# Kernel tuning notes

Hardware: AMD Instinct MI355X
Metric: run time of the kernel (lower is better)

Reference implementation:

```python
import jax, jax.numpy as jnp
import numpy as np

B, S, D_IN, D_EMB, H = 2, 2048, 1024, 1024, 16
HD = D_EMB // H

def setup_inputs() -> dict:
    key = jax.random.key(0)
    k1, k2, k3 = jax.random.split(key, 3)
    # xavier-uniform style scales
    lim_qkv = float(np.sqrt(6.0 / (D_IN + 3 * D_EMB)))
    lim_o = float(np.sqrt(6.0 / (D_EMB + D_EMB)))
    return {
        "x": jax.random.normal(k1, (B, S, D_IN), dtype=jnp.float32),
        "W_qkv": jax.random.uniform(k2, (3 * D_EMB, D_IN), minval=-lim_qkv, maxval=lim_qkv, dtype=jnp.float32),
        "b_qkv": jnp.zeros((3 * D_EMB,), dtype=jnp.float32),
        "W_o": jax.random.uniform(k3, (D_EMB, D_EMB), minval=-lim_o, maxval=lim_o, dtype=jnp.float32),
        "b_o": jnp.zeros((D_EMB,), dtype=jnp.float32),
    }

def reference(x, W_qkv, b_qkv, W_o, b_o):
    b, s, _ = x.shape
    qkv = x @ W_qkv.T + b_qkv                     # [B,S,3E]
    qkv = qkv.reshape(b, s, H, 3 * HD).transpose(0, 2, 1, 3)  # [B,H,S,3*HD]
    q, k, v = jnp.split(qkv, 3, axis=-1)          # each [B,H,S,HD]
    scale = 1.0 / np.sqrt(HD)
    attn = jax.nn.softmax(jnp.einsum('bhqd,bhkd->bhqk', q, k) * scale, axis=-1)
    vals = jnp.einsum('bhqk,bhkd->bhqd', attn, v) # [B,H,S,HD]
    vals = vals.transpose(0, 2, 1, 3).reshape(b, s, D_EMB)
    return vals @ W_o.T + b_o
```

## Files before the change

kernel.cpp:

```cpp
#include <hip/hip_runtime.h>
#include <hip/hip_bf16.h>

typedef unsigned short u16;
typedef unsigned int u32;
typedef __bf16 bf16x8 __attribute__((ext_vector_type(8)));
typedef float f32x4 __attribute__((ext_vector_type(4)));
typedef u32 u32x4 __attribute__((ext_vector_type(4)));

#define MFMA16(a, b, c) __builtin_amdgcn_mfma_f32_16x16x32_bf16((a), (b), (c), 0, 0, 0)

static __device__ __forceinline__ u16 f2bf(float f) {
  __hip_bfloat16 h = __float2bfloat16(f);
  return __builtin_bit_cast(u16, h);
}

static __device__ __forceinline__ u32 pack2(float a, float b) {
  return (u32)f2bf(a) | ((u32)f2bf(b) << 16);
}

static __device__ __forceinline__ bf16x8 ldbf8(const void* p) {
  return *reinterpret_cast<const bf16x8*>(p);
}

static __device__ __forceinline__ void gload_lds16(const void* g, void* l) {
  __builtin_amdgcn_global_load_lds(
      (const __attribute__((address_space(1))) u32*)g,
      (__attribute__((address_space(3))) u32*)l, 16, 0, 0);
}

__global__ void cvt_all(const float* __restrict__ x, const float* __restrict__ wq,
                        const float* __restrict__ wo, u16* __restrict__ xb,
                        u16* __restrict__ wqb, u16* __restrict__ wob) {
  int i = blockIdx.x * 256 + threadIdx.x;
  const float* s;
  u16* d;
  int j;
  if (i < 524288) {
    s = x; d = xb; j = i;
  } else if (i < 917504) {
    s = wq; d = wqb; j = i - 524288;
  } else {
    s = wo; d = wob; j = i - 917504;
  }
  const float4* p = reinterpret_cast<const float4*>(s) + (size_t)j * 2;
  float4 a = p[0], b = p[1];
  uint4 o;
  o.x = (u32)f2bf(a.x) | ((u32)f2bf(a.y) << 16);
  o.y = (u32)f2bf(a.z) | ((u32)f2bf(a.w) << 16);
  o.z = (u32)f2bf(b.x) | ((u32)f2bf(b.y) << 16);
  o.w = (u32)f2bf(b.z) | ((u32)f2bf(b.w) << 16);
  reinterpret_cast<uint4*>(d)[j] = o;
}

template <bool BF16OUT>
__global__ __launch_bounds__(256, 3) void gemm_bt(const u16* __restrict__ A,
                                                  const u16* __restrict__ Bm,
                                                  const float* __restrict__ bias,
                                                  void* __restrict__ Cp,
                                                  int M, int N, int K) {
  __shared__ __align__(16) char As[128 * 64 * 2];
  __shared__ __align__(16) char Bs[128 * 64 * 2];
  const int tid = threadIdx.x;
  const int lane = tid & 63;
  const int wid = tid >> 6;
  const int fr = lane & 15, fg = lane >> 4;
  const int gx = gridDim.x, nwg = gx * gridDim.y;
  const int id = blockIdx.y * gx + blockIdx.x;
  const int nid = (id & 7) * (nwg >> 3) + (id >> 3);
  const int bm = nid / gx, bn = nid % gx;
  const int wm = (wid >> 1) * 64, wn = (wid & 1) * 64;

  f32x4 acc[4][4];
#pragma unroll
  for (int i = 0; i < 4; ++i)
#pragma unroll
    for (int j = 0; j < 4; ++j) acc[i][j] = (f32x4){0.f, 0.f, 0.f, 0.f};

  const int nk = K >> 6;
  for (int kt = 0; kt < nk; ++kt) {
#pragma unroll
    for (int it = 0; it < 4; ++it) {
      int q = it * 256 + tid;
      int row = q >> 3;
      int c = (q & 7) ^ (row & 7);
      gload_lds16(A + (size_t)(bm * 128 + row) * K + kt * 64 + c * 8, As + q * 16);
      gload_lds16(Bm + (size_t)(bn * 128 + row) * K + kt * 64 + c * 8, Bs + q * 16);
    }
    __syncthreads();
#pragma unroll
    for (int mk = 0; mk < 2; ++mk) {
      bf16x8 af[4], bfr[4];
#pragma unroll
      for (int i = 0; i < 4; ++i) {
        int row = wm + i * 16 + fr;
        af[i] = ldbf8(As + ((row * 128 + mk * 64 + fg * 16) ^ ((row & 7) << 4)));
      }
#pragma unroll
      for (int j = 0; j < 4; ++j) {
        int row = wn + j * 16 + fr;
        bfr[j] = ldbf8(Bs + ((row * 128 + mk * 64 + fg * 16) ^ ((row & 7) << 4)));
      }
#pragma unroll
      for (int i = 0; i < 4; ++i)
#pragma unroll
        for (int j = 0; j < 4; ++j) acc[i][j] = MFMA16(af[i], bfr[j], acc[i][j]);
    }
    __syncthreads();
  }

#pragma unroll
  for (int j = 0; j < 4; ++j) {
    int col = bn * 128 + wn + j * 16 + fr;
    float bv = bias[col];
#pragma unroll
    for (int i = 0; i < 4; ++i) {
#pragma unroll
      for (int r = 0; r < 4; ++r) {
        int row = bm * 128 + wm + i * 16 + fg * 4 + r;
        float v = acc[i][j][r] + bv;
        if (BF16OUT)
          ((u16*)Cp)[(size_t)row * N + col] = f2bf(v);
        else
          ((float*)Cp)[(size_t)row * N + col] = v;
      }
    }
  }
}

__global__ __launch_bounds__(256, 1) void attn_fwd(const u16* __restrict__ qkv,
                                                   u16* __restrict__ aout) {
  const int id = blockIdx.y * gridDim.x + blockIdx.x;
  const int xcd = id & 7, slot = id >> 3;
  const int bh = xcd * 4 + (slot >> 3);
  const int qt = slot & 7;
  const int b = bh >> 4, h = bh & 15;
  const int tid = threadIdx.x, lane = tid & 63, wid = tid >> 6;
  const int fr = lane & 15, fg = (lane >> 4) & 3;

  __shared__ __align__(16) char Ks[2][2][64 * 128];
  __shared__ __align__(16) char VTs[2][2][64 * 128];

  const int q0 = qt * 256 + wid * 64;
  const size_t bS = (size_t)b * 2048;
  const u16* kbase = qkv + bS * 3072 + h * 192 + 64;
  const u16* vbase = qkv + bS * 3072 + h * 192 + 128;

  const int krow0 = tid >> 3, krow1 = 32 + (tid >> 3);
  const int kcol = (tid & 7) * 8;
  int kw0 = (krow0 * 128 + (tid & 7) * 16) ^ ((krow0 & 7) << 4);
  int kw1 = (krow1 * 128 + (tid & 7) * 16) ^ ((krow1 & 7) << 4);
  asm volatile("" : "+v"(kw0), "+v"(kw1));
  const int vs2 = (tid >> 3) * 2;
  const int vdc = (tid & 7) * 8;
  const int vm_ = vs2 >> 5, vG = (vs2 >> 2) & 3;
  const int vu = ((vs2 >> 4) & 1) * 2 + ((vs2 >> 1) & 1);
  const int vl0 = vm_ * 32 + ((vG ^ vu) << 3) + vu * 2;
  int wof[8];
#pragma unroll
  for (int j = 0; j < 8; ++j) {
    int d = vdc + j;
    wof[j] = ((d * 128 + vl0 * 2) ^ ((((d & 7) ^ ((d >> 3) & 7))) << 4));
    asm volatile("" : "+v"(wof[j]));
  }
  int kro[2];
#pragma unroll
  for (int mk = 0; mk < 2; ++mk) {
    kro[mk] = ((fr * 128 + mk * 64 + fg * 16) ^ ((fr & 7) << 4));
    asm volatile("" : "+v"(kro[mk]));
  }
  int vadr[4][2];
#pragma unroll
  for (int tp = 0; tp < 4; ++tp)
#pragma unroll
    for (int mk = 0; mk < 2; ++mk) {
      int d = tp * 16 + fr;
      int swz = (((d & 7) ^ ((d >> 3) & 7)) << 4);
      vadr[tp][mk] = ((d * 128 + mk * 64 + fg * 16) ^ swz);
      asm volatile("" : "+v"(vadr[tp][mk]));
    }

  bf16x8 qf[4][2];
#pragma unroll
  for (int qs = 0; qs < 4; ++qs)
#pragma unroll
    for (int mk = 0; mk < 2; ++mk) {
      bf16x8 v =
          ldbf8(qkv + (bS + q0 + qs * 16 + fr) * 3072 + h * 192 + mk * 32 + fg * 8);
#pragma unroll
      for (int e = 0; e < 8; ++e) v[e] = (__bf16)((float)v[e] * 0.1803368801f);
      qf[qs][mk] = v;
    }

  const u32 one2 = 0x3F803F80u;
  const u32x4 onev = {one2, one2, one2, one2};
  const bf16x8 onesf = __builtin_bit_cast(bf16x8, onev);
  float zs = 0.f;
  asm volatile("" : "+v"(zs));
  const f32x4 zacc = {zs, zs, zs, zs};

  f32x4 oacc[4][4];
  f32x4 lacc[4];
#pragma unroll
  for (int qs = 0; qs < 4; ++qs) {
#pragma unroll
    for (int t = 0; t < 4; ++t) oacc[qs][t] = (f32x4){0.f, 0.f, 0.f, 0.f};
    lacc[qs] = (f32x4){0.f, 0.f, 0.f, 0.f};
  }

#define LOADT(S0, K0, K1, K2, K3, V0, V1, V2, V3)                                         \
  K0 = *reinterpret_cast<const uint4*>(kbase + (size_t)((S0) + krow0) * 3072 + kcol);      \
  K1 = *reinterpret_cast<const uint4*>(kbase + (size_t)((S0) + krow1) * 3072 + kcol);      \
  K2 = *reinterpret_cast<const uint4*>(kbase + (size_t)((S0) + 64 + krow0) * 3072 + kcol); \
  K3 = *reinterpret_cast<const uint4*>(kbase + (size_t)((S0) + 64 + krow1) * 3072 + kcol); \
  V0 = *reinterpret_cast<const uint4*>(vbase + (size_t)((S0) + vs2) * 3072 + vdc);         \
  V1 = *reinterpret_cast<const uint4*>(vbase + (size_t)((S0) + vs2 + 1) * 3072 + vdc);     \
  V2 = *reinterpret_cast<const uint4*>(vbase + (size_t)((S0) + 64 + vs2) * 3072 + vdc);    \
  V3 = *reinterpret_cast<const uint4*>(vbase + (size_t)((S0) + 64 + vs2 + 1) * 3072 + vdc);

#define STAGEV1(VTP, V0, V1)                           \
  {                                                    \
    const u16* e0 = reinterpret_cast<const u16*>(&V0); \
    const u16* e1 = reinterpret_cast<const u16*>(&V1); \
    _Pragma("unroll") for (int j = 0; j < 8; ++j) {    \
      u32 w = (u32)e0[j] | ((u32)e1[j] << 16);         \
      *reinterpret_cast<u32*>((VTP) + wof[j]) = w;     \
    }                                                  \
  }

#define STAGE(BUF, K0, K1, K2, K3, V0, V1, V2, V3)        \
  {                                                       \
    *reinterpret_cast<uint4*>(Ks[BUF][0] + kw0) = K0;     \
    *reinterpret_cast<uint4*>(Ks[BUF][0] + kw1) = K1;     \
    *reinterpret_cast<uint4*>(Ks[BUF][1] + kw0) = K2;     \
    *reinterpret_cast<uint4*>(Ks[BUF][1] + kw1) = K3;     \
    STAGEV1(VTs[BUF][0], V0, V1);                         \
    STAGEV1(VTs[BUF][1], V2, V3);                         \
  }

#define BAR()                                          \
  {                                                    \
    __builtin_amdgcn_sched_barrier(0);                 \
    asm volatile("s_waitcnt lgkmcnt(0)" ::: "memory"); \
    __builtin_amdgcn_s_barrier();                      \
    __builtin_amdgcn_sched_barrier(0);                 \
  }

#define COMPUTE1(KSP, VTP)                                                     \
  {                                                                            \
    f32x4 sc[4][4];                                                            \
    __builtin_amdgcn_s_setprio(1);                                             \
    _Pragma("unroll") for (int t = 0; t < 4; ++t) {                            \
      bf16x8 kf0 = ldbf8((KSP) + kro[0] + t * 2048);                           \
      bf16x8 kf1 = ldbf8((KSP) + kro[1] + t * 2048);                           \
      _Pragma("unroll") for (int qs = 0; qs < 4; ++qs) {                       \
        sc[qs][t] = MFMA16(kf0, qf[qs][0], zacc);                              \
        sc[qs][t] = MFMA16(kf1, qf[qs][1], sc[qs][t]);                         \
      }                                                                        \
    }                                                                          \
    __builtin_amdgcn_s_setprio(0);                                             \
    u32 Wp[4][2][4];                                                           \
    _Pragma("unroll") for (int qs = 0; qs < 4; ++qs)                           \
        _Pragma("unroll") for (int t = 0; t < 4; ++t) {                        \
      Wp[qs][0][t] = pack2(__builtin_amdgcn_exp2f(sc[qs][t][0]),               \
                           __builtin_amdgcn_exp2f(sc[qs][t][1]));              \
      Wp[qs][1][t] = pack2(__builtin_amdgcn_exp2f(sc[qs][t][2]),               \
                           __builtin_amdgcn_exp2f(sc[qs][t][3]));              \
    }                                                                          \
    _Pragma("unroll") for (int mk = 0; mk < 2; ++mk) {                         \
      bf16x8 pa[4];                                                            \
      _Pragma("unroll") for (int qs = 0; qs < 4; ++qs) {                       \
        u32x4 pk;                                                              \
        pk.x = Wp[qs][0][2 * mk];                                              \
        pk.y = (u32)__shfl_xor((int)Wp[qs][1][2 * mk], 16);                    \
        pk.z = (u32)__shfl_xor((int)Wp[qs][0][2 * mk + 1], 32);                \
        pk.w = (u32)__shfl_xor((int)Wp[qs][1][2 * mk + 1], 48);                \
        pa[qs] = __builtin_bit_cast(bf16x8, pk);                               \
      }                                                                        \
      __builtin_amdgcn_s_setprio(1);                                           \
      _Pragma("unroll") for (int qs = 0; qs < 4; ++qs) lacc[qs] =              \
          MFMA16(pa[qs], onesf, lacc[qs]);                                     \
      _Pragma("unroll") for (int tp = 0; tp < 4; ++tp) {                       \
        bf16x8 vf = ldbf8((VTP) + vadr[tp][mk]);                               \
        _Pragma("unroll") for (int qs = 0; qs < 4; ++qs) oacc[qs][tp] =        \
            MFMA16(pa[qs], vf, oacc[qs][tp]);                                  \
      }                                                                        \
      __builtin_amdgcn_s_setprio(0);                                           \
    }                                                                          \
  }

#define COMPUTE(BUF)                   \
  {                                    \
    COMPUTE1(Ks[BUF][0], VTs[BUF][0]); \
    COMPUTE1(Ks[BUF][1], VTs[BUF][1]); \
  }

  uint4 ka0, ka1, ka2, ka3, va0, va1, va2, va3;
  uint4 kb0, kb1, kb2, kb3, vb0, vb1, vb2, vb3;
  LOADT(0, ka0, ka1, ka2, ka3, va0, va1, va2, va3);
  STAGE(0, ka0, ka1, ka2, ka3, va0, va1, va2, va3);
  LOADT(128, kb0, kb1, kb2, kb3, vb0, vb1, vb2, vb3);
  BAR();
  for (int kv = 0; kv < 16; kv += 2) {
    {
      int s0n = (kv + 2 < 16) ? (kv + 2) * 128 : 0;
      LOADT(s0n, ka0, ka1, ka2, ka3, va0, va1, va2, va3);
    }
    STAGE(1, kb0, kb1, kb2, kb3, vb0, vb1, vb2, vb3);
    COMPUTE(0);
    BAR();
    {
      int s0n = (kv + 3 < 16) ? (kv + 3) * 128 : 128;
      LOADT(s0n, kb0, kb1, kb2, kb3, vb0, vb1, vb2, vb3);
    }
    STAGE(0, ka0, ka1, ka2, ka3, va0, va1, va2, va3);
    COMPUTE(1);
    BAR();
  }
#undef LOADT
#undef STAGEV1
#undef STAGE
#undef BAR
#undef COMPUTE1
#undef COMPUTE

#pragma unroll
  for (int qs = 0; qs < 4; ++qs) {
    float invb[4];
#pragma unroll
    for (int r = 0; r < 4; ++r) invb[r] = 1.f / lacc[qs][r];
#pragma unroll
    for (int tp = 0; tp < 4; ++tp) {
#pragma unroll
      for (int r = 0; r < 4; ++r) {
        int row = q0 + qs * 16 + fg * 4 + r;
        aout[(bS + row) * 1024 + h * 64 + tp * 16 + fr] =
            f2bf(oacc[qs][tp][r] * invb[r]);
      }
    }
  }
}

extern "C" void kernel_launch(void* const* d_in, const int* in_sizes, int n_in,
                              void* d_out, int out_size, void* d_ws, size_t ws_size,
                              hipStream_t stream) {
  const float* x = (const float*)d_in[0];
  const float* Wqkv = (const float*)d_in[1];
  const float* bqkv = (const float*)d_in[2];
  const float* Wo = (const float*)d_in[3];
  const float* bo = (const float*)d_in[4];
  float* out = (float*)d_out;
  char* ws = (char*)d_ws;

  u16* xb = (u16*)(ws);
  u16* wqb = (u16*)(ws + 8388608);
  u16* wob = (u16*)(ws + 14680064);
  u16* qkvb = (u16*)(ws + 16777216);
  u16* attb = (u16*)(ws + 41943040);

  cvt_all<<<4096, 256, 0, stream>>>(x, Wqkv, Wo, xb, wqb, wob);

  gemm_bt<true><<<dim3(24, 32), 256, 0, stream>>>(xb, wqb, bqkv, qkvb, 4096, 3072, 1024);
  attn_fwd<<<dim3(8, 32), 256, 0, stream>>>(qkvb, attb);
  gemm_bt<false><<<dim3(8, 32), 256, 0, stream>>>(attb, wob, bo, out, 4096, 1024, 1024);
}
```

Measured before the change: 115.5 us.

## Split attention KV dimension across waves and reduce partial outputs via LDS

The attention kernel now launches twice as many blocks of 512 threads. Each block covers 128 queries, and its 8 waves form 2 query groups times 4 KV splits. Each wave processes a quarter of every KV tile, which removes the cross-lane shuffles used to build the P operand. At the end, partial O and row-sum accumulators are reduced across the 4 KV-split waves through shared memory. The aim is higher occupancy and parallelism, at the cost of redundant Q loads per wave, a final LDS reduction with extra barriers, and a smaller per-wave MFMA workload.

```diff
diff --git a/kernel.cpp b/kernel.cpp
--- a/kernel.cpp
+++ b/kernel.cpp
@@ -127,57 +127,53 @@
   }
 }
 
-__global__ __launch_bounds__(256, 1) void attn_fwd(const u16* __restrict__ qkv,
+__global__ __launch_bounds__(512, 2) void attn_fwd(const u16* __restrict__ qkv,
                                                    u16* __restrict__ aout) {
   const int id = blockIdx.y * gridDim.x + blockIdx.x;
   const int xcd = id & 7, slot = id >> 3;
-  const int bh = xcd * 4 + (slot >> 3);
-  const int qt = slot & 7;
+  const int bh = xcd * 4 + (slot >> 4);
+  const int qt = slot & 15;
   const int b = bh >> 4, h = bh & 15;
   const int tid = threadIdx.x, lane = tid & 63, wid = tid >> 6;
   const int fr = lane & 15, fg = (lane >> 4) & 3;
-
-  __shared__ __align__(16) char Ks[2][2][64 * 128];
-  __shared__ __align__(16) char VTs[2][2][64 * 128];
-
-  const int q0 = qt * 256 + wid * 64;
+  const int kw = wid & 3, qw = wid >> 2;
+
+  __shared__ __align__(16) char smem[65536];
+
+  const int q0 = qt * 128 + qw * 64;
   const size_t bS = (size_t)b * 2048;
   const u16* kbase = qkv + bS * 3072 + h * 192 + 64;
   const u16* vbase = qkv + bS * 3072 + h * 192 + 128;
 
-  const int krow0 = tid >> 3, krow1 = 32 + (tid >> 3);
-  const int kcol = (tid & 7) * 8;
-  int kw0 = (krow0 * 128 + (tid & 7) * 16) ^ ((krow0 & 7) << 4);
-  int kw1 = (krow1 * 128 + (tid & 7) * 16) ^ ((krow1 & 7) << 4);
-  asm volatile("" : "+v"(kw0), "+v"(kw1));
-  const int vs2 = (tid >> 3) * 2;
+  const int kr = tid >> 2, c4 = tid & 3;
+  int kwo0 = (kr * 128 + c4 * 16) ^ ((kr & 7) << 4);
+  int kwo1 = (kr * 128 + (c4 + 4) * 16) ^ ((kr & 7) << 4);
+  asm volatile("" : "+v"(kwo0), "+v"(kwo1));
+  const int p2 = (tid >> 3) * 2;
   const int vdc = (tid & 7) * 8;
-  const int vm_ = vs2 >> 5, vG = (vs2 >> 2) & 3;
-  const int vu = ((vs2 >> 4) & 1) * 2 + ((vs2 >> 1) & 1);
-  const int vl0 = vm_ * 32 + ((vG ^ vu) << 3) + vu * 2;
+  const int pp = p2 & 31;
+  const int vl0 = (p2 & ~31) + ((pp >> 2) & 3) * 8 + ((pp >> 4) & 1) * 4 + (pp & 3);
   int wof[8];
 #pragma unroll
   for (int j = 0; j < 8; ++j) {
     int d = vdc + j;
-    wof[j] = ((d * 128 + vl0 * 2) ^ ((((d & 7) ^ ((d >> 3) & 7))) << 4));
+    wof[j] = 32768 + ((d * 256 + vl0 * 2) ^ ((((d & 7) ^ ((d >> 3) & 7))) << 4));
     asm volatile("" : "+v"(wof[j]));
   }
   int kro[2];
 #pragma unroll
   for (int mk = 0; mk < 2; ++mk) {
-    kro[mk] = ((fr * 128 + mk * 64 + fg * 16) ^ ((fr & 7) << 4));
+    kro[mk] = kw * 4096 + ((fr * 128 + mk * 64 + fg * 16) ^ ((fr & 7) << 4));
     asm volatile("" : "+v"(kro[mk]));
   }
-  int vadr[4][2];
-#pragma unroll
-  for (int tp = 0; tp < 4; ++tp)
-#pragma unroll
-    for (int mk = 0; mk < 2; ++mk) {
-      int d = tp * 16 + fr;
-      int swz = (((d & 7) ^ ((d >> 3) & 7)) << 4);
-      vadr[tp][mk] = ((d * 128 + mk * 64 + fg * 16) ^ swz);
-      asm volatile("" : "+v"(vadr[tp][mk]));
-    }
+  int vadr[4];
+#pragma unroll
+  for (int tp = 0; tp < 4; ++tp) {
+    int d = tp * 16 + fr;
+    vadr[tp] =
+        32768 + ((d * 256 + kw * 64 + fg * 16) ^ ((((d & 7) ^ ((d >> 3) & 7))) << 4));
+    asm volatile("" : "+v"(vadr[tp]));
+  }
 
   bf16x8 qf[4][2];
 #pragma unroll
@@ -207,34 +203,23 @@
     lacc[qs] = (f32x4){0.f, 0.f, 0.f, 0.f};
   }
 
-#define LOADT(S0, K0, K1, K2, K3, V0, V1, V2, V3)                                         \
-  K0 = *reinterpret_cast<const uint4*>(kbase + (size_t)((S0) + krow0) * 3072 + kcol);      \
-  K1 = *reinterpret_cast<const uint4*>(kbase + (size_t)((S0) + krow1) * 3072 + kcol);      \
-  K2 = *reinterpret_cast<const uint4*>(kbase + (size_t)((S0) + 64 + krow0) * 3072 + kcol); \
-  K3 = *reinterpret_cast<const uint4*>(kbase + (size_t)((S0) + 64 + krow1) * 3072 + kcol); \
-  V0 = *reinterpret_cast<const uint4*>(vbase + (size_t)((S0) + vs2) * 3072 + vdc);         \
-  V1 = *reinterpret_cast<const uint4*>(vbase + (size_t)((S0) + vs2 + 1) * 3072 + vdc);     \
-  V2 = *reinterpret_cast<const uint4*>(vbase + (size_t)((S0) + 64 + vs2) * 3072 + vdc);    \
-  V3 = *reinterpret_cast<const uint4*>(vbase + (size_t)((S0) + 64 + vs2 + 1) * 3072 + vdc);
-
-#define STAGEV1(VTP, V0, V1)                           \
-  {                                                    \
-    const u16* e0 = reinterpret_cast<const u16*>(&V0); \
-    const u16* e1 = reinterpret_cast<const u16*>(&V1); \
-    _Pragma("unroll") for (int j = 0; j < 8; ++j) {    \
-      u32 w = (u32)e0[j] | ((u32)e1[j] << 16);         \
-      *reinterpret_cast<u32*>((VTP) + wof[j]) = w;     \
-    }                                                  \
-  }
-
-#define STAGE(BUF, K0, K1, K2, K3, V0, V1, V2, V3)        \
-  {                                                       \
-    *reinterpret_cast<uint4*>(Ks[BUF][0] + kw0) = K0;     \
-    *reinterpret_cast<uint4*>(Ks[BUF][0] + kw1) = K1;     \
-    *reinterpret_cast<uint4*>(Ks[BUF][1] + kw0) = K2;     \
-    *reinterpret_cast<uint4*>(Ks[BUF][1] + kw1) = K3;     \
-    STAGEV1(VTs[BUF][0], V0, V1);                         \
-    STAGEV1(VTs[BUF][1], V2, V3);                         \
+#define LOADT(S0, K0, K1, V0, V1)                                                   \
+  K0 = *reinterpret_cast<const uint4*>(kbase + (size_t)((S0) + kr) * 3072 + c4 * 8); \
+  K1 = *reinterpret_cast<const uint4*>(kbase + (size_t)((S0) + kr) * 3072 +          \
+                                       (c4 + 4) * 8);                                \
+  V0 = *reinterpret_cast<const uint4*>(vbase + (size_t)((S0) + p2) * 3072 + vdc);    \
+  V1 = *reinterpret_cast<const uint4*>(vbase + (size_t)((S0) + p2 + 1) * 3072 + vdc);
+
+#define STAGE(BUF, K0, K1, V0, V1)                               \
+  {                                                              \
+    *reinterpret_cast<uint4*>(smem + (BUF)*16384 + kwo0) = K0;   \
+    *reinterpret_cast<uint4*>(smem + (BUF)*16384 + kwo1) = K1;   \
+    const u16* e0 = reinterpret_cast<const u16*>(&V0);           \
+    const u16* e1 = reinterpret_cast<const u16*>(&V1);           \
+    _Pragma("unroll") for (int j = 0; j < 8; ++j) {              \
+      u32 w = (u32)e0[j] | ((u32)e1[j] << 16);                   \
+      *reinterpret_cast<u32*>(smem + (BUF)*16384 + wof[j]) = w;  \
+    }                                                            \
   }
 
 #define BAR()                                          \
@@ -245,96 +230,128 @@
     __builtin_amdgcn_sched_barrier(0);                 \
   }
 
-#define COMPUTE1(KSP, VTP)                                                     \
+#define COMPUTE(BUF)                                                           \
   {                                                                            \
-    f32x4 sc[4][4];                                                            \
+    f32x4 sc[2][4];                                                            \
     __builtin_amdgcn_s_setprio(1);                                             \
-    _Pragma("unroll") for (int t = 0; t < 4; ++t) {                            \
-      bf16x8 kf0 = ldbf8((KSP) + kro[0] + t * 2048);                           \
-      bf16x8 kf1 = ldbf8((KSP) + kro[1] + t * 2048);                           \
+    _Pragma("unroll") for (int ks = 0; ks < 2; ++ks) {                         \
+      bf16x8 kf0 = ldbf8(smem + (BUF)*16384 + kro[0] + ks * 2048);             \
+      bf16x8 kf1 = ldbf8(smem + (BUF)*16384 + kro[1] + ks * 2048);             \
       _Pragma("unroll") for (int qs = 0; qs < 4; ++qs) {                       \
-        sc[qs][t] = MFMA16(kf0, qf[qs][0], zacc);                              \
-        sc[qs][t] = MFMA16(kf1, qf[qs][1], sc[qs][t]);                         \
+        sc[ks][qs] = MFMA16(kf0, qf[qs][0], zacc);                             \
+        sc[ks][qs] = MFMA16(kf1, qf[qs][1], sc[ks][qs]);                       \
       }                                                                        \
     }                                                                          \
     __builtin_amdgcn_s_setprio(0);                                             \
-    u32 Wp[4][2][4];                                                           \
-    _Pragma("unroll") for (int qs = 0; qs < 4; ++qs)                           \
-        _Pragma("unroll") for (int t = 0; t < 4; ++t) {                        \
-      Wp[qs][0][t] = pack2(__builtin_amdgcn_exp2f(sc[qs][t][0]),               \
-                           __builtin_amdgcn_exp2f(sc[qs][t][1]));              \
-      Wp[qs][1][t] = pack2(__builtin_amdgcn_exp2f(sc[qs][t][2]),               \
-                           __builtin_amdgcn_exp2f(sc[qs][t][3]));              \
+    bf16x8 pa[4];                                                              \
+    _Pragma("unroll") for (int qs = 0; qs < 4; ++qs) {                         \
+      u32x4 pk;                                                                \
+      pk.x = pack2(__builtin_amdgcn_exp2f(sc[0][qs][0]),                       \
+                   __builtin_amdgcn_exp2f(sc[0][qs][1]));                      \
+      pk.y = pack2(__builtin_amdgcn_exp2f(sc[0][qs][2]),                       \
+                   __builtin_amdgcn_exp2f(sc[0][qs][3]));                      \
+      pk.z = pack2(__builtin_amdgcn_exp2f(sc[1][qs][0]),                       \
+                   __builtin_amdgcn_exp2f(sc[1][qs][1]));                      \
+      pk.w = pack2(__builtin_amdgcn_exp2f(sc[1][qs][2]),                       \
+                   __builtin_amdgcn_exp2f(sc[1][qs][3]));                      \
+      pa[qs] = __builtin_bit_cast(bf16x8, pk);                                 \
     }                                                                          \
-    _Pragma("unroll") for (int mk = 0; mk < 2; ++mk) {                         \
-      bf16x8 pa[4];                                                            \
-      _Pragma("unroll") for (int qs = 0; qs < 4; ++qs) {                       \
-        u32x4 pk;                                                              \
-        pk.x = Wp[qs][0][2 * mk];                                              \
-        pk.y = (u32)__shfl_xor((int)Wp[qs][1][2 * mk], 16);                    \
-        pk.z = (u32)__shfl_xor((int)Wp[qs][0][2 * mk + 1], 32);                \
-        pk.w = (u32)__shfl_xor((int)Wp[qs][1][2 * mk + 1], 48);                \
-        pa[qs] = __builtin_bit_cast(bf16x8, pk);                               \
-      }                                                                        \
-      __builtin_amdgcn_s_setprio(1);                                           \
-      _Pragma("unroll") for (int qs = 0; qs < 4; ++qs) lacc[qs] =              \
-          MFMA16(pa[qs], onesf, lacc[qs]);                                     \
-      _Pragma("unroll") for (int tp = 0; tp < 4; ++tp) {                       \
-        bf16x8 vf = ldbf8((VTP) + vadr[tp][mk]);                               \
-        _Pragma("unroll") for (int qs = 0; qs < 4; ++qs) oacc[qs][tp] =        \
-            MFMA16(pa[qs], vf, oacc[qs][tp]);                                  \
-      }                                                                        \
-      __builtin_amdgcn_s_setprio(0);                                           \
+    __builtin_amdgcn_s_setprio(1);                                             \
+    _Pragma("unroll") for (int qs = 0; qs < 4; ++qs) lacc[qs] =                \
+        MFMA16(pa[qs], onesf, lacc[qs]);                                       \
+    _Pragma("unroll") for (int tp = 0; tp < 4; ++tp) {                         \
+      bf16x8 vf = ldbf8(smem + (BUF)*16384 + vadr[tp]);                        \
+      _Pragma("unroll") for (int qs = 0; qs < 4; ++qs) oacc[qs][tp] =          \
+          MFMA16(pa[qs], vf, oacc[qs][tp]);                                    \
     }                                                                          \
-  }
-
-#define COMPUTE(BUF)                   \
-  {                                    \
-    COMPUTE1(Ks[BUF][0], VTs[BUF][0]); \
-    COMPUTE1(Ks[BUF][1], VTs[BUF][1]); \
-  }
-
-  uint4 ka0, ka1, ka2, ka3, va0, va1, va2, va3;
-  uint4 kb0, kb1, kb2, kb3, vb0, vb1, vb2, vb3;
-  LOADT(0, ka0, ka1, ka2, ka3, va0, va1, va2, va3);
-  STAGE(0, ka0, ka1, ka2, ka3, va0, va1, va2, va3);
-  LOADT(128, kb0, kb1, kb2, kb3, vb0, vb1, vb2, vb3);
+    __builtin_amdgcn_s_setprio(0);                                             \
+  }
+
+  uint4 ka0, ka1, va0, va1;
+  uint4 kb0, kb1, vb0, vb1;
+  LOADT(0, ka0, ka1, va0, va1);
+  STAGE(0, ka0, ka1, va0, va1);
+  LOADT(128, kb0, kb1, vb0, vb1);
   BAR();
   for (int kv = 0; kv < 16; kv += 2) {
     {
       int s0n = (kv + 2 < 16) ? (kv + 2) * 128 : 0;
-      LOADT(s0n, ka0, ka1, ka2, ka3, va0, va1, va2, va3);
-    }
-    STAGE(1, kb0, kb1, kb2, kb3, vb0, vb1, vb2, vb3);
+      LOADT(s0n, ka0, ka1, va0, va1);
+    }
+    STAGE(1, kb0, kb1, vb0, vb1);
     COMPUTE(0);
     BAR();
     {
       int s0n = (kv + 3 < 16) ? (kv + 3) * 128 : 128;
-      LOADT(s0n, kb0, kb1, kb2, kb3, vb0, vb1, vb2, vb3);
-    }
-    STAGE(0, ka0, ka1, ka2, ka3, va0, va1, va2, va3);
+      LOADT(s0n, kb0, kb1, vb0, vb1);
+    }
+    STAGE(0, ka0, ka1, va0, va1);
     COMPUTE(1);
     BAR();
   }
 #undef LOADT
-#undef STAGEV1
 #undef STAGE
+#undef COMPUTE
+
+  f32x4 fin[4];
+  f32x4 lfin;
+#pragma unroll
+  for (int tp = 0; tp < 4; ++tp) fin[tp] = oacc[0][tp];
+  lfin = lacc[0];
+#pragma unroll
+  for (int qs = 1; qs < 4; ++qs) {
+    bool own = (qs == kw);
+#pragma unroll
+    for (int tp = 0; tp < 4; ++tp) fin[tp] = own ? oacc[qs][tp] : fin[tp];
+    lfin = own ? lacc[qs] : lfin;
+  }
+  const int lofs = lane * 16;
+#pragma unroll
+  for (int rr = 0; rr < 2; ++rr) {
+#pragma unroll
+    for (int qs = 0; qs < 4; ++qs)
+#pragma unroll
+      for (int tpo = 0; tpo < 2; ++tpo)
+        *reinterpret_cast<f32x4*>(
+            smem + (((qw * 4 + qs) * 4 + kw) * 2 + tpo) * 1024 + lofs) =
+            oacc[qs][rr * 2 + tpo];
+    BAR();
+#pragma unroll
+    for (int w2 = 0; w2 < 4; ++w2) {
+      if (w2 != kw) {
+#pragma unroll
+        for (int tpo = 0; tpo < 2; ++tpo)
+          fin[rr * 2 + tpo] += *reinterpret_cast<const f32x4*>(
+              smem + (((qw * 4 + kw) * 4 + w2) * 2 + tpo) * 1024 + lofs);
+      }
+    }
+    BAR();
+  }
+#pragma unroll
+  for (int qs = 0; qs < 4; ++qs)
+    *reinterpret_cast<f32x4*>(smem + ((qw * 4 + qs) * 4 + kw) * 1024 + lofs) =
+        lacc[qs];
+  BAR();
+#pragma unroll
+  for (int w2 = 0; w2 < 4; ++w2) {
+    if (w2 != kw) {
+      lfin += *reinterpret_cast<const f32x4*>(
+          smem + ((qw * 4 + kw) * 4 + w2) * 1024 + lofs);
+    }
+  }
 #undef BAR
-#undef COMPUTE1
-#undef COMPUTE
-
-#pragma unroll
-  for (int qs = 0; qs < 4; ++qs) {
+
+  {
     float invb[4];
 #pragma unroll
-    for (int r = 0; r < 4; ++r) invb[r] = 1.f / lacc[qs][r];
+    for (int r = 0; r < 4; ++r) invb[r] = 1.f / lfin[r];
 #pragma unroll
     for (int tp = 0; tp < 4; ++tp) {
 #pragma unroll
       for (int r = 0; r < 4; ++r) {
-        int row = q0 + qs * 16 + fg * 4 + r;
+        int row = q0 + kw * 16 + fg * 4 + r;
         aout[(bS + row) * 1024 + h * 64 + tp * 16 + fr] =
-            f2bf(oacc[qs][tp][r] * invb[r]);
+            f2bf(fin[tp][r] * invb[r]);
       }
     }
   }
@@ -360,6 +377,6 @@
   cvt_all<<<4096, 256, 0, stream>>>(x, Wqkv, Wo, xb, wqb, wob);
 
   gemm_bt<true><<<dim3(24, 32), 256, 0, stream>>>(xb, wqb, bqkv, qkvb, 4096, 3072, 1024);
-  attn_fwd<<<dim3(8, 32), 256, 0, stream>>>(qkvb, attb);
+  attn_fwd<<<dim3(16, 32), 512, 0, stream>>>(qkvb, attb);
   gemm_bt<false><<<dim3(8, 32), 256, 0, stream>>>(attb, wob, bo, out, 4096, 1024, 1024);
 }
```

After: 112.8 us. 2.4% less time.
